# Optimization experiments

Measured on AMD Instinct MI355X. Metric: run time of the kernel, lower is better.

## Reference

```python
import jax, jax.numpy as jnp
import numpy as np

N = 10000
E = 160000
D = 512
EPS = 1e-5


def _lin_params(key, out_d, in_d, bias=True):
    k1, k2 = jax.random.split(key)
    s = 1.0 / np.sqrt(in_d)
    W = jax.random.uniform(k1, (out_d, in_d), jnp.float32, -s, s)
    if bias:
        b = jax.random.uniform(k2, (out_d,), jnp.float32, -s, s)
        return W, b
    return (W,)


def setup_inputs() -> dict:
    key = jax.random.key(0)
    ks = jax.random.split(key, 16)
    inp = {
        "x": jax.random.normal(ks[0], (N, D), jnp.float32),
        "edge_index": jax.random.randint(ks[1], (2, E), 0, N, jnp.int64),
    }
    ki = 2
    for l in range(3):
        Wp, bp = _lin_params(ks[ki], D, D); ki += 1
        Wl, bl = _lin_params(ks[ki], D, D); ki += 1
        (Wr,) = _lin_params(ks[ki], D, D, bias=False); ki += 1
        inp[f"Wp{l}"] = Wp; inp[f"bp{l}"] = bp
        inp[f"Wl{l}"] = Wl; inp[f"bl{l}"] = bl
        inp[f"Wr{l}"] = Wr
        if l < 2:  # ReLU+LayerNorm between convs
            inp[f"g{l}"] = jnp.ones((D,), jnp.float32)
            inp[f"be{l}"] = jnp.zeros((D,), jnp.float32)
    return inp


def _sage_conv(x, src, dst, Wp, bp, Wl, bl, Wr):
    # PyG SAGEConv with project=True: project+ReLU messages, mean-aggregate, lin_l + lin_r(root)
    h = jax.nn.relu(x @ Wp.T + bp)                      # [N, D] projected messages
    agg = jax.ops.segment_sum(h[src], dst, num_segments=N)   # gather + scatter-add
    cnt = jax.ops.segment_sum(jnp.ones((src.shape[0],), x.dtype), dst, num_segments=N)
    agg = agg / jnp.maximum(cnt, 1.0)[:, None]          # mean over incoming edges
    return agg @ Wl.T + bl + x @ Wr.T


def _relu_ln(x, g, b):
    x = jax.nn.relu(x)
    mu = jnp.mean(x, axis=-1, keepdims=True)
    var = jnp.mean(jnp.square(x - mu), axis=-1, keepdims=True)
    return (x - mu) * jax.lax.rsqrt(var + EPS) * g + b


def reference(x, edge_index,
              Wp0, bp0, Wl0, bl0, Wr0, g0, be0,
              Wp1, bp1, Wl1, bl1, Wr1, g1, be1,
              Wp2, bp2, Wl2, bl2, Wr2):
    src, dst = edge_index[0], edge_index[1]
    x = _sage_conv(x, src, dst, Wp0, bp0, Wl0, bl0, Wr0)
    x = _relu_ln(x, g0, be0)
    x = _sage_conv(x, src, dst, Wp1, bp1, Wl1, bl1, Wr1)
    x = _relu_ln(x, g1, be1)
    x = _sage_conv(x, src, dst, Wp2, bp2, Wl2, bl2, Wr2)
    return x
```

## Files before the change

kernel.cpp:

```cpp
#include <hip/hip_runtime.h>
#include <cstdint>

#define D 512
#define TM 128
#define TN 64
#define BK 32
#define CAP 64

typedef unsigned short u16;
typedef __bf16 bf16x8 __attribute__((ext_vector_type(8)));
typedef float f32x4 __attribute__((ext_vector_type(4)));

__device__ __forceinline__ float bf2f(u16 u) {
    unsigned int x = ((unsigned int)u) << 16;
    return __builtin_bit_cast(float, x);
}
__device__ __forceinline__ u16 f2bf(float f) {
    unsigned int x = __builtin_bit_cast(unsigned int, f);
    x += 0x7fffu + ((x >> 16) & 1u);
    return (u16)(x >> 16);
}

__global__ void detect(const u16* __restrict__ xraw, const int* __restrict__ eraw,
                       int* __restrict__ flags)
{
    __shared__ int cf, ci;
    if (threadIdx.x == 0) { cf = 0; ci = 0; }
    __syncthreads();
    int t = threadIdx.x;
    u16 u = xraw[2 * t];
    int e = (u >> 7) & 0xFF;
    if (e >= 110 && e <= 129) atomicAdd(&cf, 1);
    if (eraw[2 * t + 1] == 0) atomicAdd(&ci, 1);
    __syncthreads();
    if (threadIdx.x == 0) {
        flags[0] = (cf >= 128) ? 1 : 0;
        flags[1] = (ci >= 128) ? 1 : 0;
    }
}

__global__ __launch_bounds__(256) void convert_x(
    const void* __restrict__ src, u16* __restrict__ out, const int* __restrict__ flags)
{
    int i = (blockIdx.x * 256 + threadIdx.x) * 8;
    if (flags[0]) {
        *(uint4*)(out + i) = *(const uint4*)((const u16*)src + i);
    } else {
        const float* f = (const float*)src + i;
        float4 a = *(const float4*)f;
        float4 b = *(const float4*)(f + 4);
        u16 r[8] = {f2bf(a.x), f2bf(a.y), f2bf(a.z), f2bf(a.w),
                    f2bf(b.x), f2bf(b.y), f2bf(b.z), f2bf(b.w)};
        *(uint4*)(out + i) = *(uint4*)r;
    }
}

struct Ptrs9  { const void* p[9];  };
struct Ptrs10 { const void* p[10]; };

__global__ __launch_bounds__(256) void convert_mat(
    Ptrs9 s, u16* __restrict__ out, const int* __restrict__ flags)
{
    int m = blockIdx.y;
    const void* src = s.p[m];
    u16* o = out + (size_t)m * D * D;
    int i = (blockIdx.x * 256 + threadIdx.x) * 8;
    if (flags[0]) {
        *(uint4*)(o + i) = *(const uint4*)((const u16*)src + i);
    } else {
        const float* f = (const float*)src + i;
        float4 a = *(const float4*)f;
        float4 b = *(const float4*)(f + 4);
        u16 r[8] = {f2bf(a.x), f2bf(a.y), f2bf(a.z), f2bf(a.w),
                    f2bf(b.x), f2bf(b.y), f2bf(b.z), f2bf(b.w)};
        *(uint4*)(o + i) = *(uint4*)r;
    }
}

__global__ __launch_bounds__(256) void convert_vec(
    Ptrs10 s, float* __restrict__ out, const int* __restrict__ flags)
{
    int b = blockIdx.x;
    const void* src = s.p[b];
#pragma unroll
    for (int j = threadIdx.x * 2; j < threadIdx.x * 2 + 2; j++) {
        float v = flags[0] ? bf2f(((const u16*)src)[j]) : ((const float*)src)[j];
        out[b * 512 + j] = v;
    }
}

__global__ __launch_bounds__(256) void convert_edges(
    const int* __restrict__ eraw, int* __restrict__ esrc, int* __restrict__ edst,
    const int* __restrict__ flags, int E, int Nn)
{
    int e = blockIdx.x * 256 + threadIdx.x;
    if (e >= E) return;
    int s, d;
    if (flags[1]) { s = eraw[2 * e]; d = eraw[2 * (E + e)]; }
    else          { s = eraw[e];     d = eraw[E + e]; }
    esrc[e] = min(max(s, 0), Nn - 1);
    edst[e] = min(max(d, 0), Nn - 1);
}

template <int NPASS, bool RELU, bool FINAL>
__global__ __launch_bounds__(256) void gemm_bt(
    const u16* __restrict__ A0, const u16* __restrict__ B0,
    const u16* __restrict__ A1, const u16* __restrict__ B1,
    const float* __restrict__ bias, void* __restrict__ Cout,
    const int* __restrict__ flags, int M)
{
    __shared__ __align__(16) u16 sA[TM * BK];
    __shared__ __align__(16) u16 sB[TN * BK];

    const int t    = threadIdx.x;
    const int m0   = blockIdx.x * TM;
    const int n0   = blockIdx.y * TN;
    const int wave = t >> 6, lane = t & 63;
    const int wm   = wave >> 1, wn = wave & 1;
    const int lrow = lane & 15, quad = lane >> 4;

    f32x4 acc[4][2];
#pragma unroll
    for (int i = 0; i < 4; i++)
#pragma unroll
        for (int j = 0; j < 2; j++)
#pragma unroll
            for (int r = 0; r < 4; r++) acc[i][j][r] = 0.f;

    const int cA    = (t & 3) * 8;
    const int rowA0 = min(m0 + (t >> 2),      M - 1);
    const int rowA1 = min(m0 + 64 + (t >> 2), M - 1);
    const int rowB  = n0 + (t >> 2);

#pragma unroll 1
    for (int p = 0; p < NPASS; p++) {
        const u16* A = p ? A1 : A0;
        const u16* B = p ? B1 : B0;
        const u16* gA0 = A + (size_t)rowA0 * D + cA;
        const u16* gA1 = A + (size_t)rowA1 * D + cA;
        const u16* gB  = B + (size_t)rowB  * D + cA;

#pragma unroll 1
        for (int k0 = 0; k0 < D; k0 += BK) {
            uint4 va0 = *(const uint4*)(gA0 + k0);
            uint4 va1 = *(const uint4*)(gA1 + k0);
            uint4 vb  = *(const uint4*)(gB  + k0);
            __syncthreads();
            *(uint4*)&sA[(size_t)t * 8]         = va0;
            *(uint4*)&sA[(size_t)(t + 256) * 8] = va1;
            *(uint4*)&sB[(size_t)t * 8]         = vb;
            __syncthreads();

            bf16x8 af[4], bfr[2];
#pragma unroll
            for (int mi = 0; mi < 4; mi++) {
                int r = wm * 64 + mi * 16 + lrow;
                af[mi] = *(const bf16x8*)&sA[r * BK + quad * 8];
            }
#pragma unroll
            for (int ni = 0; ni < 2; ni++) {
                int r = wn * 32 + ni * 16 + lrow;
                bfr[ni] = *(const bf16x8*)&sB[r * BK + quad * 8];
            }
#pragma unroll
            for (int mi = 0; mi < 4; mi++)
#pragma unroll
                for (int ni = 0; ni < 2; ni++)
                    acc[mi][ni] = __builtin_amdgcn_mfma_f32_16x16x32_bf16(
                        af[mi], bfr[ni], acc[mi][ni], 0, 0, 0);
        }
    }

    const int out_bf16 = FINAL ? flags[0] : 1;
#pragma unroll
    for (int ni = 0; ni < 2; ni++) {
        int col = n0 + wn * 32 + ni * 16 + lrow;
        float bv = bias[col];
#pragma unroll
        for (int mi = 0; mi < 4; mi++) {
            int row0 = m0 + wm * 64 + mi * 16 + quad * 4;
#pragma unroll
            for (int r = 0; r < 4; r++) {
                int row = row0 + r;
                if (row < M) {
                    float v = acc[mi][ni][r] + bv;
                    if (RELU) v = fmaxf(v, 0.f);
                    if (!FINAL || out_bf16)
                        ((u16*)Cout)[(size_t)row * D + col] = f2bf(v);
                    else
                        ((float*)Cout)[(size_t)row * D + col] = v;
                }
            }
        }
    }
}

__global__ void build_bucket(const int* __restrict__ esrc, const int* __restrict__ edst,
                             int* __restrict__ cnt, u16* __restrict__ bucket, int E)
{
    int e = blockIdx.x * 256 + threadIdx.x;
    if (e < E) {
        int d = edst[e];
        int p = atomicAdd(&cnt[d], 1);
        if (p < CAP) bucket[(size_t)d * CAP + p] = (u16)esrc[e];
    }
}

__global__ __launch_bounds__(256) void aggregate(
    const u16* __restrict__ h, const int* __restrict__ cnt,
    const u16* __restrict__ bucket, u16* __restrict__ agg)
{
    const int n = blockIdx.x;
    const int t = threadIdx.x;
    const int deg = cnt[n];
    const int dd  = min(deg, CAP);

    __shared__ u16 sidx[CAP];
    if (t < dd) sidx[t] = bucket[(size_t)n * CAP + t];
    __syncthreads();

    float a0 = 0.f, a1 = 0.f;
    for (int i = 0; i < dd; i++) {
        int s = sidx[i];
        unsigned int v = *(const unsigned int*)(h + (size_t)s * D + t * 2);
        a0 += bf2f((u16)(v & 0xffffu));
        a1 += bf2f((u16)(v >> 16));
    }
    float inv = 1.f / fmaxf((float)deg, 1.f);
    unsigned int o = (unsigned int)f2bf(a0 * inv) | ((unsigned int)f2bf(a1 * inv) << 16);
    *(unsigned int*)(agg + (size_t)n * D + t * 2) = o;
}

__global__ __launch_bounds__(256) void relu_ln(
    const u16* __restrict__ y, const float* __restrict__ g, const float* __restrict__ be,
    u16* __restrict__ out, int M)
{
    const int row  = blockIdx.x * 4 + (threadIdx.x >> 6);
    const int lane = threadIdx.x & 63;
    if (row >= M) return;

    typedef short s16x8 __attribute__((ext_vector_type(8)));
    s16x8 v = *(const s16x8*)(y + (size_t)row * D + lane * 8);
    float f[8], s = 0.f, s2 = 0.f;
#pragma unroll
    for (int i = 0; i < 8; i++) {
        float x = bf2f((u16)v[i]);
        x = fmaxf(x, 0.f);
        f[i] = x; s += x; s2 += x * x;
    }
#pragma unroll
    for (int off = 32; off >= 1; off >>= 1) {
        s  += __shfl_xor(s, off);
        s2 += __shfl_xor(s2, off);
    }
    float mean = s * (1.f / 512.f);
    float var  = s2 * (1.f / 512.f) - mean * mean;
    float rstd = rsqrtf(var + 1e-5f);

    s16x8 res;
#pragma unroll
    for (int i = 0; i < 8; i++) {
        float o = (f[i] - mean) * rstd * g[lane * 8 + i] + be[lane * 8 + i];
        res[i] = (short)f2bf(o);
    }
    *(s16x8*)(out + (size_t)row * D + lane * 8) = res;
}

extern "C" void kernel_launch(void* const* d_in, const int* in_sizes, int n_in,
                              void* d_out, int out_size, void* d_ws, size_t ws_size,
                              hipStream_t stream)
{
    const int M = in_sizes[0] / D;
    const int E = in_sizes[1] / 2;
    const void* xraw = d_in[0];
    const int*  eraw = (const int*)d_in[1];

    const void *Wp[3], *bp[3], *Wl[3], *bl[3], *Wr[3], *g[2], *be[2];
    int idx = 2;
    for (int l = 0; l < 3; l++) {
        Wp[l] = d_in[idx++]; bp[l] = d_in[idx++];
        Wl[l] = d_in[idx++]; bl[l] = d_in[idx++];
        Wr[l] = d_in[idx++];
        if (l < 2) { g[l] = d_in[idx++]; be[l] = d_in[idx++]; }
    }

    char* w = (char*)d_ws;
    auto alloc = [&](size_t bytes) { void* p = w; w += (bytes + 255) & ~(size_t)255; return p; };
    u16*   xb     = (u16*)  alloc((size_t)M * D * 2);
    u16*   h      = (u16*)  alloc((size_t)M * D * 2);
    u16*   agg    = (u16*)  alloc((size_t)M * D * 2);
    u16*   Wb     = (u16*)  alloc((size_t)9 * D * D * 2);
    float* vecf   = (float*)alloc((size_t)10 * 512 * 4);
    int*   esrc   = (int*)  alloc((size_t)E * 4);
    int*   edst   = (int*)  alloc((size_t)E * 4);
    int*   cnt    = (int*)  alloc((size_t)M * 4);
    u16*   bucket = (u16*)  alloc((size_t)M * CAP * 2);
    int*   flags  = (int*)  alloc(256);

    detect<<<1, 256, 0, stream>>>((const u16*)xraw, eraw, flags);

    convert_x<<<dim3(M * D / (256 * 8)), dim3(256), 0, stream>>>(xraw, xb, flags);

    Ptrs9 mats;
    const void* morder[9] = {Wp[0], Wl[0], Wr[0], Wp[1], Wl[1], Wr[1], Wp[2], Wl[2], Wr[2]};
    for (int i = 0; i < 9; i++) mats.p[i] = morder[i];
    convert_mat<<<dim3(D * D / (256 * 8), 9), dim3(256), 0, stream>>>(mats, Wb, flags);

    Ptrs10 vecs;
    const void* vorder[10] = {bp[0], bl[0], g[0], be[0], bp[1], bl[1], g[1], be[1], bp[2], bl[2]};
    for (int i = 0; i < 10; i++) vecs.p[i] = vorder[i];
    convert_vec<<<dim3(10), dim3(256), 0, stream>>>(vecs, vecf, flags);

    convert_edges<<<dim3((E + 255) / 256), dim3(256), 0, stream>>>(eraw, esrc, edst, flags, E, M);

    hipMemsetAsync(cnt, 0, (size_t)M * 4, stream);
    build_bucket<<<dim3((E + 255) / 256), dim3(256), 0, stream>>>(esrc, edst, cnt, bucket, E);

    const u16* WM[9]; for (int i = 0; i < 9; i++) WM[i] = Wb + (size_t)i * D * D;
    const float* VB[10]; for (int i = 0; i < 10; i++) VB[i] = vecf + (size_t)i * 512;

    u16* yb = (u16*)d_out;
    dim3 gg((M + TM - 1) / TM, D / TN);
    const u16* xin = xb;
    for (int l = 0; l < 3; l++) {
        gemm_bt<1, true, false><<<gg, dim3(256), 0, stream>>>(
            xin, WM[l * 3 + 0], xin, WM[l * 3 + 0], VB[l * 4 + 0], h, flags, M);
        aggregate<<<dim3(M), dim3(256), 0, stream>>>(h, cnt, bucket, agg);
        if (l < 2) {
            gemm_bt<2, false, false><<<gg, dim3(256), 0, stream>>>(
                agg, WM[l * 3 + 1], xin, WM[l * 3 + 2], VB[l * 4 + 1], yb, flags, M);
            relu_ln<<<dim3((M + 3) / 4), dim3(256), 0, stream>>>(
                yb, VB[l * 4 + 2], VB[l * 4 + 3], xb, M);
            xin = xb;
        } else {
            gemm_bt<2, false, true><<<gg, dim3(256), 0, stream>>>(
                agg, WM[l * 3 + 1], xin, WM[l * 3 + 2], VB[l * 4 + 1], d_out, flags, M);
        }
    }
}
```

Measured before the change: 377.9 us.

## Use direct global-to-LDS loads in GEMM and wave-per-node vectorized aggregation

```diff
diff --git a/kernel.cpp b/kernel.cpp
--- a/kernel.cpp
+++ b/kernel.cpp
@@ -19,6 +19,13 @@
     unsigned int x = __builtin_bit_cast(unsigned int, f);
     x += 0x7fffu + ((x >> 16) & 1u);
     return (u16)(x >> 16);
+}
+
+__device__ __forceinline__ void gload16(const u16* g, u16* l) {
+    __builtin_amdgcn_global_load_lds(
+        (const __attribute__((address_space(1))) void*)(uintptr_t)g,
+        (__attribute__((address_space(3))) void*)(unsigned int)(uintptr_t)l,
+        16, 0, 0);
 }
 
 __global__ void detect(const u16* __restrict__ xraw, const int* __restrict__ eraw,
@@ -142,13 +149,9 @@
 
 #pragma unroll 1
         for (int k0 = 0; k0 < D; k0 += BK) {
-            uint4 va0 = *(const uint4*)(gA0 + k0);
-            uint4 va1 = *(const uint4*)(gA1 + k0);
-            uint4 vb  = *(const uint4*)(gB  + k0);
-            __syncthreads();
-            *(uint4*)&sA[(size_t)t * 8]         = va0;
-            *(uint4*)&sA[(size_t)(t + 256) * 8] = va1;
-            *(uint4*)&sB[(size_t)t * 8]         = vb;
+            gload16(gA0 + k0, &sA[(size_t)t * 8]);
+            gload16(gA1 + k0, &sA[(size_t)(t + 256) * 8]);
+            gload16(gB  + k0, &sB[(size_t)t * 8]);
             __syncthreads();
 
             bf16x8 af[4], bfr[2];
@@ -168,6 +171,7 @@
                 for (int ni = 0; ni < 2; ni++)
                     acc[mi][ni] = __builtin_amdgcn_mfma_f32_16x16x32_bf16(
                         af[mi], bfr[ni], acc[mi][ni], 0, 0, 0);
+            __syncthreads();
         }
     }
 
@@ -208,27 +212,51 @@
 
 __global__ __launch_bounds__(256) void aggregate(
     const u16* __restrict__ h, const int* __restrict__ cnt,
-    const u16* __restrict__ bucket, u16* __restrict__ agg)
-{
-    const int n = blockIdx.x;
-    const int t = threadIdx.x;
-    const int deg = cnt[n];
-    const int dd  = min(deg, CAP);
-
-    __shared__ u16 sidx[CAP];
-    if (t < dd) sidx[t] = bucket[(size_t)n * CAP + t];
+    const u16* __restrict__ bucket, u16* __restrict__ agg, int M)
+{
+    const int w = threadIdx.x >> 6, lane = threadIdx.x & 63;
+    const int n = blockIdx.x * 4 + w;
+
+    __shared__ u16 sidx[4][CAP];
+    int deg = 0, dd = 0;
+    if (n < M) {
+        deg = cnt[n];
+        dd  = min(deg, CAP);
+        if (lane < dd) sidx[w][lane] = bucket[(size_t)n * CAP + lane];
+    }
     __syncthreads();
-
-    float a0 = 0.f, a1 = 0.f;
-    for (int i = 0; i < dd; i++) {
-        int s = sidx[i];
-        unsigned int v = *(const unsigned int*)(h + (size_t)s * D + t * 2);
-        a0 += bf2f((u16)(v & 0xffffu));
-        a1 += bf2f((u16)(v >> 16));
-    }
+    if (n >= M) return;
+
+    float a[8] = {0.f, 0.f, 0.f, 0.f, 0.f, 0.f, 0.f, 0.f};
+    int i = 0;
+    for (; i + 2 <= dd; i += 2) {
+        int s0 = sidx[w][i], s1 = sidx[w][i + 1];
+        uint4 v0 = *(const uint4*)(h + (size_t)s0 * D + lane * 8);
+        uint4 v1 = *(const uint4*)(h + (size_t)s1 * D + lane * 8);
+        const unsigned int* u0 = (const unsigned int*)&v0;
+        const unsigned int* u1 = (const unsigned int*)&v1;
+#pragma unroll
+        for (int j = 0; j < 4; j++) {
+            a[2 * j]     += bf2f((u16)(u0[j] & 0xffffu)) + bf2f((u16)(u1[j] & 0xffffu));
+            a[2 * j + 1] += bf2f((u16)(u0[j] >> 16))     + bf2f((u16)(u1[j] >> 16));
+        }
+    }
+    if (i < dd) {
+        int s0 = sidx[w][i];
+        uint4 v0 = *(const uint4*)(h + (size_t)s0 * D + lane * 8);
+        const unsigned int* u0 = (const unsigned int*)&v0;
+#pragma unroll
+        for (int j = 0; j < 4; j++) {
+            a[2 * j]     += bf2f((u16)(u0[j] & 0xffffu));
+            a[2 * j + 1] += bf2f((u16)(u0[j] >> 16));
+        }
+    }
+
     float inv = 1.f / fmaxf((float)deg, 1.f);
-    unsigned int o = (unsigned int)f2bf(a0 * inv) | ((unsigned int)f2bf(a1 * inv) << 16);
-    *(unsigned int*)(agg + (size_t)n * D + t * 2) = o;
+    u16 r[8];
+#pragma unroll
+    for (int j = 0; j < 8; j++) r[j] = f2bf(a[j] * inv);
+    *(uint4*)(agg + (size_t)n * D + lane * 8) = *(uint4*)r;
 }
 
 __global__ __launch_bounds__(256) void relu_ln(
@@ -325,7 +353,7 @@
     for (int l = 0; l < 3; l++) {
         gemm_bt<1, true, false><<<gg, dim3(256), 0, stream>>>(
             xin, WM[l * 3 + 0], xin, WM[l * 3 + 0], VB[l * 4 + 0], h, flags, M);
-        aggregate<<<dim3(M), dim3(256), 0, stream>>>(h, cnt, bucket, agg);
+        aggregate<<<dim3((M + 3) / 4), dim3(256), 0, stream>>>(h, cnt, bucket, agg, M);
         if (l < 2) {
             gemm_bt<2, false, false><<<gg, dim3(256), 0, stream>>>(
                 agg, WM[l * 3 + 1], xin, WM[l * 3 + 2], VB[l * 4 + 1], yb, flags, M);
```

After: 368.6 us. 2.5% less time.
